# Kernel tuning notes

Hardware: AMD Instinct MI355X
Metric: run time of the kernel (lower is better)

Reference implementation:

```python
import jax, jax.numpy as jnp
import numpy as np

N0, N1 = 20000, 20000     # users, items
F0 = 512                  # raw feature dim per type
HID = 64                  # hidden_dim == H * D
H, D = 8, 8               # num_heads, out_dim
P = 2                     # metapaths per side
E = 200000                # metapath instances per metapath
L = 3                     # metapath length (nodes)
B = 8192                  # link-prediction target batch
AV = 128                  # attn_vec_dim
CH = 128                  # ProductMLP hidden = max(128, HID//2)
ETYPES_USER = [[0, 1], [0, 1]]
ETYPES_ITEM = [[1, 0], [1, 0]]


def setup_inputs() -> dict:
    key = jax.random.key(0)
    ks = jax.random.split(key, 32)
    def nrm(k, shape, fan_in):
        return (jax.random.normal(k, shape, dtype=jnp.float32) * (1.414 / np.sqrt(fan_in))).astype(jnp.float32)
    inp = {}
    inp['feats0'] = jax.random.normal(ks[0], (N0, F0), dtype=jnp.float32)
    inp['feats1'] = jax.random.normal(ks[1], (N1, F0), dtype=jnp.float32)
    for t, off in ((0, 2), (1, 6)):
        inp[f'tower{t}_pw'] = nrm(ks[off], (F0, HID), F0)
        inp[f'tower{t}_pb'] = jnp.zeros((HID,), jnp.float32)
        inp[f'tower{t}_w2'] = nrm(ks[off + 1], (HID, HID), HID)
        inp[f'tower{t}_b2'] = jnp.zeros((HID,), jnp.float32)
        inp[f'tower{t}_g'] = jnp.ones((HID,), jnp.float32)
        inp[f'tower{t}_be'] = jnp.zeros((HID,), jnp.float32)
    inp['r_vec'] = jax.random.normal(ks[10], (2, HID // 2, 2), dtype=jnp.float32)
    inp['attn_user'] = nrm(ks[11], (P, H, D), D)
    inp['attn_item'] = nrm(ks[12], (P, H, D), D)
    inp['su_w1'] = nrm(ks[13], (HID, AV), HID)
    inp['su_b1'] = jnp.zeros((AV,), jnp.float32)
    inp['su_w2'] = nrm(ks[14], (AV,), AV)
    inp['si_w1'] = nrm(ks[15], (HID, AV), HID)
    inp['si_b1'] = jnp.zeros((AV,), jnp.float32)
    inp['si_w2'] = nrm(ks[16], (AV,), AV)
    inp['cw1'] = nrm(ks[17], (HID, CH), HID)
    inp['cb1'] = jnp.zeros((CH,), jnp.float32)
    inp['cw2'] = nrm(ks[18], (CH, 2), CH)
    inp['idx0'] = jnp.arange(N0, dtype=jnp.int32)
    inp['idx1'] = jnp.arange(N1, dtype=jnp.int32) + N0
    inp['emi_user'] = jax.random.randint(ks[20], (P, E, L), 0, N0 + N1, dtype=jnp.int32)
    inp['tgt_user'] = jax.random.randint(ks[21], (P, E), 0, B, dtype=jnp.int32)
    inp['emi_item'] = jax.random.randint(ks[22], (P, E, L), 0, N0 + N1, dtype=jnp.int32)
    inp['tgt_item'] = jax.random.randint(ks[23], (P, E), 0, B, dtype=jnp.int32)
    return inp


def _tower(x, pw, pb, w2, b2, g, be):
    # Linear -> GELU -> Linear -> residual -> LayerNorm (dropout off in eval)
    z = x @ pw + pb
    h = jax.nn.gelu(z, approximate=False)
    h = h @ w2 + b2
    y = h + z
    mu = y.mean(-1, keepdims=True)
    var = ((y - mu) ** 2).mean(-1, keepdims=True)
    return (y - mu) / jnp.sqrt(var + 1e-5) * g + be


def _rot_full(r_vec):
    # normalize to unit complex, then even etypes = r, odd etypes = conj(r)
    r = r_vec / jnp.linalg.norm(r_vec, axis=-1, keepdims=True)
    conj = r * jnp.array([1.0, -1.0], dtype=r.dtype)
    return jnp.stack([r, conj], axis=1).reshape(-1, r.shape[1], 2)  # [num_edge_type, HID//2, 2]


def _final_r(rfull, etypes):
    # cumulative complex rotation applied to each position along the metapath
    fr = [None] * L
    fr[L - 1] = jnp.stack([jnp.ones(HID // 2), jnp.zeros(HID // 2)], axis=1).astype(rfull.dtype)
    for i in range(L - 2, -1, -1):
        rv = rfull[etypes[i]]
        re = fr[i + 1][:, 0] * rv[:, 0] - fr[i + 1][:, 1] * rv[:, 1]
        im = fr[i + 1][:, 0] * rv[:, 1] + fr[i + 1][:, 1] * rv[:, 0]
        fr[i] = jnp.stack([re, im], axis=1)
    return jnp.stack(fr)  # [L, HID//2, 2]


def _metapath(feat, emi, tgt, attn, etypes, rfull):
    # gather node features along each metapath instance: [E, L, HID//2, 2]
    ed = feat[emi].reshape(emi.shape[0], L, HID // 2, 2)
    fr = _final_r(rfull, etypes)  # last position is identity rotation
    re = ed[..., 0] * fr[:, :, 0] - ed[..., 1] * fr[:, :, 1]
    im = ed[..., 0] * fr[:, :, 1] + ed[..., 1] * fr[:, :, 0]
    hidden = jnp.stack([re, im], -1).mean(axis=1).reshape(-1, HID)  # mean over metapath positions
    eft = hidden.reshape(-1, H, D)
    e = jax.nn.leaky_relu((eft * attn).sum(-1), 0.01)  # [E, H]
    # edge softmax over instances sharing a target node
    m = jax.ops.segment_max(e, tgt, num_segments=B)
    m = jnp.where(jnp.isfinite(m), m, 0.0)
    a = jnp.exp(e - m[tgt])
    s = jax.ops.segment_sum(a, tgt, num_segments=B)
    w = a / (s[tgt] + 1e-9)
    ret = jax.ops.segment_sum(w[..., None] * eft, tgt, num_segments=B)  # [B, H, D]
    return jax.nn.elu(ret.reshape(B, HID))


def _semantic(outs, w1, b1, w2):
    hs = jnp.stack(outs)  # [P, B, HID]
    s = (jnp.tanh(hs @ w1 + b1) @ w2).mean(axis=1)  # [P]
    beta = jax.nn.softmax(s)
    return (beta[:, None, None] * hs).sum(0)  # [B, HID]


def reference(feats0, feats1, tower0_pw, tower0_pb, tower0_w2, tower0_b2, tower0_g, tower0_be,
              tower1_pw, tower1_pb, tower1_w2, tower1_b2, tower1_g, tower1_be,
              r_vec, attn_user, attn_item, su_w1, su_b1, su_w2, si_w1, si_b1, si_w2,
              cw1, cb1, cw2, idx0, idx1, emi_user, tgt_user, emi_item, tgt_item):
    t0 = _tower(feats0, tower0_pw, tower0_pb, tower0_w2, tower0_b2, tower0_g, tower0_be)
    t1 = _tower(feats1, tower1_pw, tower1_pb, tower1_w2, tower1_b2, tower1_g, tower1_be)
    feat = jnp.zeros((N0 + N1, HID), jnp.float32).at[idx0].set(t0).at[idx1].set(t1)
    rfull = _rot_full(r_vec)
    user_outs = [_metapath(feat, emi_user[p], tgt_user[p], attn_user[p], ETYPES_USER[p], rfull) for p in range(P)]
    item_outs = [_metapath(feat, emi_item[p], tgt_item[p], attn_item[p], ETYPES_ITEM[p], rfull) for p in range(P)]
    h_user = _semantic(user_outs, su_w1, su_b1, su_w2)
    h_item = _semantic(item_outs, si_w1, si_b1, si_w2)
    x = h_user * h_item
    h = jax.nn.relu(x @ cw1 + cb1)
    logits = h @ cw2
    return jax.nn.softmax(logits, axis=-1)
```

## Files before the change

kernel.cpp:

```cpp
#include <hip/hip_runtime.h>
#include <hip/hip_bf16.h>
#include <math.h>

#define NN0 20000
#define NN1 20000
#define NTOT 40000
#define FF0 512
#define HIDD 64
#define EEE 200000
#define BBB 8192
#define AVV 128
#define CHH 128

typedef __bf16 bf16x8 __attribute__((ext_vector_type(8)));
typedef __bf16 bf16x4 __attribute__((ext_vector_type(4)));
typedef float f32x4 __attribute__((ext_vector_type(4)));
typedef float f32x2 __attribute__((ext_vector_type(2)));

__device__ __forceinline__ float fast_tanh(float x) {
    float e2 = __expf(2.f * x);
    return 1.f - 2.f / (e2 + 1.f);
}

__device__ __forceinline__ f32x2 bf2_to_f32x2(unsigned int c) {
    f32x2 r;
    r.x = __uint_as_float(c << 16);
    r.y = __uint_as_float(c & 0xffff0000u);
    return r;
}

__global__ __launch_bounds__(256) void prep_hist(
    const float* __restrict__ pw0, const float* __restrict__ pw1,
    const float* __restrict__ w20, const float* __restrict__ w21,
    __bf16* __restrict__ wprep, __bf16* __restrict__ w2prep,
    const int* __restrict__ tgt_user, const int* __restrict__ tgt_item,
    int* __restrict__ cnt)
{
    int bx = blockIdx.x;
    if (bx < 16) {
        int tw = bx & 1, seg = bx >> 1;
        const float* w = tw ? pw1 : pw0;
        __bf16* base = wprep + tw * 65536;
        for (int idx = seg * 4096 + threadIdx.x; idx < (seg + 1) * 4096; idx += 256) {
            int k = idx >> 6, n = idx & 63;
            float v = w[idx];
            __bf16 hi = (__bf16)v;
            __bf16 lo = (__bf16)(v - (float)hi);
            int ks = k >> 5, kb = (k >> 3) & 3, j = k & 7;
            int nt = n >> 4, fr = n & 15;
            int lane = kb * 16 + fr;
            int off = ((ks * 4 + nt) * 64 + lane) * 8 + j;
            base[off] = hi;
            base[32768 + off] = lo;
        }
        const float* w2 = tw ? w21 : w20;
        __bf16* base2 = w2prep + tw * 8192;
        for (int idx = seg * 512 + threadIdx.x; idx < (seg + 1) * 512; idx += 256) {
            int k = idx >> 6, n = idx & 63;
            float v = w2[idx];
            __bf16 hi = (__bf16)v;
            __bf16 lo = (__bf16)(v - (float)hi);
            int ks = k >> 5, kb = (k >> 3) & 3, j = k & 7;
            int nt = n >> 4, fr = n & 15;
            int lane = kb * 16 + fr;
            int off = ((ks * 4 + nt) * 64 + lane) * 8 + j;
            base2[off] = hi;
            base2[4096 + off] = lo;
        }
    } else {
        int flat = bx - 16;
        int combo = flat & 3, blk = flat >> 2;
        const int* tgt = (combo < 2 ? tgt_user : tgt_item) + (long)(combo & 1) * EEE;
        int i = blk * 256 + threadIdx.x;
        if (i < EEE) atomicAdd(&cnt[combo * BBB + tgt[i]], 1);
    }
}

__global__ __launch_bounds__(256) void scan_kernel(const int* __restrict__ cnt, int* __restrict__ offs,
                                                   int* __restrict__ cur32, float* __restrict__ s_acc)
{
    int pth = blockIdx.x;
    if (pth == 0 && threadIdx.x < 4) s_acc[threadIdx.x] = 0.f;
    const int* c = cnt + pth * BBB;
    int* o = offs + pth * (BBB + 1);
    __shared__ int part[256];
    int tid = threadIdx.x;
    int base = tid * 32;
    int local[32];
    int sum = 0;
    for (int j = 0; j < 32; j++) { local[j] = sum; sum += c[base + j]; }
    part[tid] = sum;
    __syncthreads();
    for (int d = 1; d < 256; d <<= 1) {
        int v = (tid >= d) ? part[tid - d] : 0;
        __syncthreads();
        part[tid] += v;
        __syncthreads();
    }
    int pre = (tid == 0) ? 0 : part[tid - 1];
    for (int j = 0; j < 32; j++) {
        int val = pre + local[j];
        o[base + j] = val;
        if (((base + j) & 255) == 0) cur32[pth * 32 + ((base + j) >> 8)] = val;
    }
    if (tid == 255) o[BBB] = pre + sum;
}

#define CHUNKF 1024
__global__ __launch_bounds__(128) void tower_binA(
    const float* __restrict__ x0, const float* __restrict__ x1,
    const __bf16* __restrict__ wprep, const __bf16* __restrict__ w2prep,
    const float* __restrict__ pb0, const float* __restrict__ pb1,
    const float* __restrict__ b20, const float* __restrict__ b21,
    const float* __restrict__ g0, const float* __restrict__ g1,
    const float* __restrict__ be0, const float* __restrict__ be1,
    const int* __restrict__ idxa, const int* __restrict__ idxb,
    __hip_bfloat16* __restrict__ feat,
    const int* __restrict__ tgt_user, const int* __restrict__ tgt_item,
    const int* __restrict__ emi_user, const int* __restrict__ emi_item,
    int* __restrict__ cur32, ushort4* __restrict__ binbuf)
{
    __shared__ __align__(16) char pool[8960];
    int bx = blockIdx.x;
    if (bx < 2500) {
        int tile = bx >> 1, tw = bx & 1;
        const float* x  = tw ? x1 : x0;
        const float* pb = tw ? pb1 : pb0;
        const float* b2 = tw ? b21 : b20;
        const float* g  = tw ? g1 : g0;
        const float* be = tw ? be1 : be0;
        const int* idx  = tw ? idxb : idxa;
        float (*hs)[68] = (float(*)[68])pool;
        float* pq  = (float*)(pool + 4352);
        float* pq2 = (float*)(pool + 4480);

        int wv = threadIdx.x >> 6;
        int l = threadIdx.x & 63;
        int fr = l & 15, kb = l >> 4;
        int nt0 = 2 * wv;
        int row0 = tile * 16;
        const float* xp = x + (long)(row0 + fr) * FF0 + kb * 8;
        const __bf16* bp = wprep + tw * 65536;

        f32x4 acc[2];
#pragma unroll
        for (int n2 = 0; n2 < 2; n2++) acc[n2] = (f32x4){0.f, 0.f, 0.f, 0.f};

        float4 a0c, a1c, a0n, a1n;
        bf16x8 bhc[2], blc[2], bhn[2], bln[2];

        a0c = *(const float4*)xp;
        a1c = *(const float4*)(xp + 4);
#pragma unroll
        for (int n2 = 0; n2 < 2; n2++) {
            bhc[n2] = *(const bf16x8*)(bp + ((nt0 + n2) * 64 + l) * 8);
            blc[n2] = *(const bf16x8*)(bp + 32768 + ((nt0 + n2) * 64 + l) * 8);
        }

#pragma unroll 2
        for (int ks = 0; ks < 16; ks++) {
            if (ks + 1 < 16) {
                a0n = *(const float4*)(xp + (ks + 1) * 32);
                a1n = *(const float4*)(xp + (ks + 1) * 32 + 4);
#pragma unroll
                for (int n2 = 0; n2 < 2; n2++) {
                    bhn[n2] = *(const bf16x8*)(bp + (((ks + 1) * 4 + nt0 + n2) * 64 + l) * 8);
                    bln[n2] = *(const bf16x8*)(bp + 32768 + (((ks + 1) * 4 + nt0 + n2) * 64 + l) * 8);
                }
            }
            float av[8] = {a0c.x, a0c.y, a0c.z, a0c.w, a1c.x, a1c.y, a1c.z, a1c.w};
            bf16x8 ah, al;
#pragma unroll
            for (int j = 0; j < 8; j++) {
                __bf16 h = (__bf16)av[j];
                ah[j] = h;
                al[j] = (__bf16)(av[j] - (float)h);
            }
#pragma unroll
            for (int n2 = 0; n2 < 2; n2++) {
                acc[n2] = __builtin_amdgcn_mfma_f32_16x16x32_bf16(ah, bhc[n2], acc[n2], 0, 0, 0);
                acc[n2] = __builtin_amdgcn_mfma_f32_16x16x32_bf16(al, bhc[n2], acc[n2], 0, 0, 0);
                acc[n2] = __builtin_amdgcn_mfma_f32_16x16x32_bf16(ah, blc[n2], acc[n2], 0, 0, 0);
            }
            a0c = a0n; a1c = a1n;
#pragma unroll
            for (int n2 = 0; n2 < 2; n2++) { bhc[n2] = bhn[n2]; blc[n2] = bln[n2]; }
        }

        float pbv[2], b2v[2];
#pragma unroll
        for (int n2 = 0; n2 < 2; n2++) {
            pbv[n2] = pb[(nt0 + n2) * 16 + fr];
            b2v[n2] = b2[(nt0 + n2) * 16 + fr];
        }
        f32x4 acc2[2];
#pragma unroll
        for (int n2 = 0; n2 < 2; n2++) {
#pragma unroll
            for (int j = 0; j < 4; j++) {
                float z = acc[n2][j] + pbv[n2];
                float h = 0.5f * z * (1.f + erff(z * 0.70710678118654752f));
                hs[kb * 4 + j][(nt0 + n2) * 16 + fr] = h;
                acc2[n2][j] = z + b2v[n2];
            }
        }
        __syncthreads();

        const __bf16* w2p = w2prep + tw * 8192;
#pragma unroll
        for (int ks = 0; ks < 2; ks++) {
            float4 h0 = *(const float4*)&hs[fr][ks * 32 + kb * 8];
            float4 h1 = *(const float4*)&hs[fr][ks * 32 + kb * 8 + 4];
            float hv[8] = {h0.x, h0.y, h0.z, h0.w, h1.x, h1.y, h1.z, h1.w};
            bf16x8 ah, al;
#pragma unroll
            for (int j = 0; j < 8; j++) {
                __bf16 h = (__bf16)hv[j];
                ah[j] = h;
                al[j] = (__bf16)(hv[j] - (float)h);
            }
#pragma unroll
            for (int n2 = 0; n2 < 2; n2++) {
                bf16x8 bh2 = *(const bf16x8*)(w2p + ((ks * 4 + nt0 + n2) * 64 + l) * 8);
                bf16x8 bl2 = *(const bf16x8*)(w2p + 4096 + ((ks * 4 + nt0 + n2) * 64 + l) * 8);
                acc2[n2] = __builtin_amdgcn_mfma_f32_16x16x32_bf16(ah, bh2, acc2[n2], 0, 0, 0);
                acc2[n2] = __builtin_amdgcn_mfma_f32_16x16x32_bf16(al, bh2, acc2[n2], 0, 0, 0);
                acc2[n2] = __builtin_amdgcn_mfma_f32_16x16x32_bf16(ah, bl2, acc2[n2], 0, 0, 0);
            }
        }

        float pj[4];
#pragma unroll
        for (int j = 0; j < 4; j++) {
            float p = acc2[0][j] + acc2[1][j];
            p += __shfl_xor(p, 1); p += __shfl_xor(p, 2);
            p += __shfl_xor(p, 4); p += __shfl_xor(p, 8);
            pj[j] = p;
        }
        if (fr == 0) {
#pragma unroll
            for (int j = 0; j < 4; j++) pq[wv * 16 + kb * 4 + j] = pj[j];
        }
        __syncthreads();
        float mu[4];
#pragma unroll
        for (int j = 0; j < 4; j++)
            mu[j] = (pj[j] + pq[(wv ^ 1) * 16 + kb * 4 + j]) * (1.f / 64.f);
        float d[2][4], vj[4];
#pragma unroll
        for (int j = 0; j < 4; j++) {
            d[0][j] = acc2[0][j] - mu[j];
            d[1][j] = acc2[1][j] - mu[j];
            float v = d[0][j] * d[0][j] + d[1][j] * d[1][j];
            v += __shfl_xor(v, 1); v += __shfl_xor(v, 2);
            v += __shfl_xor(v, 4); v += __shfl_xor(v, 8);
            vj[j] = v;
        }
        if (fr == 0) {
#pragma unroll
            for (int j = 0; j < 4; j++) pq2[wv * 16 + kb * 4 + j] = vj[j];
        }
        __syncthreads();
        float gv[2], bev[2];
#pragma unroll
        for (int n2 = 0; n2 < 2; n2++) {
            gv[n2] = g[(nt0 + n2) * 16 + fr];
            bev[n2] = be[(nt0 + n2) * 16 + fr];
        }
#pragma unroll
        for (int j = 0; j < 4; j++) {
            float var = (vj[j] + pq2[(wv ^ 1) * 16 + kb * 4 + j]) * (1.f / 64.f);
            float is = 1.f / sqrtf(var + 1e-5f);
#pragma unroll
            for (int n2 = 0; n2 < 2; n2++)
                hs[kb * 4 + j][(nt0 + n2) * 16 + fr] = d[n2][j] * is * gv[n2] + bev[n2];
        }
        __syncthreads();
#pragma unroll
        for (int r = 0; r < 8; r++) {
            int rr = wv * 8 + r;
            feat[(long)idx[row0 + rr] * HIDD + l] = __float2bfloat16(hs[rr][l]);
        }
    } else {
        int flat = bx - 2500;
        int combo = flat & 3;
        int base = (flat >> 2) * CHUNKF;
        const int* tgt = (combo < 2 ? tgt_user : tgt_item) + (long)(combo & 1) * EEE;
        const int* emi = (combo < 2 ? emi_user : emi_item) + (long)(combo & 1) * EEE * 3;
        ushort4* sbuf = (ushort4*)pool;
        int* lcnt  = (int*)(pool + 8192);
        int* lofs  = lcnt + 32;
        int* gbase = lofs + 33;
        int* lcur  = gbase + 32;
        int tid = threadIdx.x;
        if (tid < 32) { lcnt[tid] = 0; lcur[tid] = 0; }
        __syncthreads();
        ushort4 ent[8]; int bk[8];
#pragma unroll
        for (int ps = 0; ps < 8; ps++) {
            int i = base + ps * 128 + tid;
            if (i < EEE) {
                int t = tgt[i];
                ent[ps] = make_ushort4((unsigned short)emi[3 * i], (unsigned short)emi[3 * i + 1],
                                       (unsigned short)emi[3 * i + 2], (unsigned short)t);
                bk[ps] = t >> 8;
                atomicAdd(&lcnt[bk[ps]], 1);
            } else bk[ps] = -1;
        }
        __syncthreads();
        if (tid == 0) {
            int run = 0;
            for (int k = 0; k < 32; k++) { lofs[k] = run; run += lcnt[k]; }
            lofs[32] = run;
        }
        __syncthreads();
        if (tid < 32) gbase[tid] = atomicAdd(&cur32[combo * 32 + tid], lcnt[tid]);
        __syncthreads();
#pragma unroll
        for (int ps = 0; ps < 8; ps++) {
            if (bk[ps] >= 0) {
                int pos = lofs[bk[ps]] + atomicAdd(&lcur[bk[ps]], 1);
                sbuf[pos] = ent[ps];
            }
        }
        __syncthreads();
        int total = lofs[32];
        ushort4* dst = binbuf + (long)combo * EEE;
        for (int j = tid; j < total; j += 128) {
            ushort4 e = sbuf[j];
            int k = e.w >> 8;
            dst[gbase[k] + (j - lofs[k])] = e;
        }
    }
}

#define BKCAP 7680
__global__ __launch_bounds__(256) void binB_kernel(
    const int* __restrict__ offs,
    const ushort4* __restrict__ binbuf, ushort4* __restrict__ nodes)
{
    int combo = blockIdx.y;
    int k = blockIdx.x;
    const int* of = offs + combo * (BBB + 1);
    int rbeg = of[k << 8], rend = of[(k + 1) << 8];
    int cnt = rend - rbeg;
    if (cnt > BKCAP) cnt = BKCAP;
    __shared__ ushort4 sbuf[BKCAP];
    __shared__ int lh[256];
    __shared__ int part[256];
    int tid = threadIdx.x;
    lh[tid] = 0;
    __syncthreads();
    const ushort4* src = binbuf + (long)combo * EEE + rbeg;
    for (int j = tid; j < cnt; j += 256)
        atomicAdd(&lh[src[j].w & 255], 1);
    __syncthreads();
    int myc = lh[tid];
    part[tid] = myc;
    __syncthreads();
    for (int d = 1; d < 256; d <<= 1) {
        int u = (tid >= d) ? part[tid - d] : 0;
        __syncthreads();
        part[tid] += u;
        __syncthreads();
    }
    int myofs = part[tid] - myc;
    __syncthreads();
    lh[tid] = myofs;
    part[tid] = 0;
    __syncthreads();
    for (int j = tid; j < cnt; j += 256) {
        ushort4 e = src[j];
        int b = e.w & 255;
        int pos = lh[b] + atomicAdd(&part[b], 1);
        if (pos < BKCAP) sbuf[pos] = e;
    }
    __syncthreads();
    ushort4* dst = nodes + (long)combo * EEE + rbeg;
    for (int j = tid; j < cnt; j += 256) dst[j] = sbuf[j];
}

__global__ __launch_bounds__(256) void flash_mp(
    const __hip_bfloat16* __restrict__ feat, const ushort4* __restrict__ nodes,
    const int* __restrict__ offs, const float* __restrict__ r_vec,
    const float* __restrict__ attn_user, const float* __restrict__ attn_item,
    float* __restrict__ ret)
{
    int combo = blockIdx.y;
    int wid = threadIdx.x >> 6, lane = threadIdx.x & 63;
    int half = lane >> 5, p = lane & 31;
    int side = combo >> 1;
    const float* attn = (side == 0 ? attn_user : attn_item) + (combo & 1) * 64;
    const unsigned int* f2 = (const unsigned int*)feat;
    float2 rb = ((const float2*)r_vec)[p];
    float invn = 1.f / sqrtf(rb.x * rb.x + rb.y * rb.y);
    float rvx = rb.x * invn, rvy = rb.y * invn;
    if (side == 0) rvy = -rvy;
    float aRe = attn[2 * p], aIm = attn[2 * p + 1];
    f32x2 av  = { aRe * (1.f / 3.f), aIm * (1.f / 3.f) };
    f32x2 apv = { (rvx * aRe + rvy * aIm) * (1.f / 3.f),
                  (rvx * aIm - rvy * aRe) * (1.f / 3.f) };
    int t = blockIdx.x * 4 + wid;
    const int* of = offs + combo * (BBB + 1);
    int beg = of[t], end = of[t + 1];
    int n = end - beg;
    const ushort4* nd = nodes + (long)combo * EEE;

    float m = -3.4e38f, s = 0.f;
    f32x2 A02 = {0.f, 0.f}, A1 = {0.f, 0.f};

    unsigned int c0[4], c1[4], c2[4];
    ushort4 nq[4];
    if (n > 0) {
#pragma unroll
        for (int q = 0; q < 4; q++) {
            ushort4 a = nd[min(beg + 2 * q + half, EEE - 1)];
            c0[q] = f2[(int)a.x * 32 + p];
            c1[q] = f2[(int)a.y * 32 + p];
            c2[q] = f2[(int)a.z * 32 + p];
        }
#pragma unroll
        for (int q = 0; q < 4; q++)
            nq[q] = nd[min(beg + 8 + 2 * q + half, EEE - 1)];
    }
    for (int it = 0; it < n; it += 8) {
        f32x2 u1[4], v02[4];
        float e[4];
#pragma unroll
        for (int q = 0; q < 4; q++) {
            f32x2 u0 = bf2_to_f32x2(c0[q]);
            u1[q]    = bf2_to_f32x2(c1[q]);
            f32x2 u2 = bf2_to_f32x2(c2[q]);
            v02[q] = u0 + u2;
        }
        if (it + 8 < n) {
#pragma unroll
            for (int q = 0; q < 4; q++) {
                c0[q] = f2[(int)nq[q].x * 32 + p];
                c1[q] = f2[(int)nq[q].y * 32 + p];
                c2[q] = f2[(int)nq[q].z * 32 + p];
            }
#pragma unroll
            for (int q = 0; q < 4; q++)
                nq[q] = nd[min(beg + it + 16 + 2 * q + half, EEE - 1)];
        }
#pragma unroll
        for (int q = 0; q < 4; q++) {
            f32x2 tt = v02[q] * av + u1[q] * apv;
            float pa = tt.x + tt.y;
            pa += __shfl_xor(pa, 1);
            pa += __shfl_xor(pa, 2);
            e[q] = fmaxf(pa, 0.01f * pa);
        }
        if (it + 8 > n) {
#pragma unroll
            for (int q = 0; q < 4; q++)
                if (it + 2 * q + half >= n) e[q] = -3.4e38f;
        }
        float mx = fmaxf(fmaxf(e[0], e[1]), fmaxf(e[2], e[3]));
        float mn = fmaxf(m, fmaxf(mx, __shfl_xor(mx, 32)));
        float alpha = __expf(m - mn);
        s *= alpha; A02 *= alpha; A1 *= alpha;
        float wl = 0.f;
#pragma unroll
        for (int q = 0; q < 4; q++) {
            float w = __expf(e[q] - mn);
            wl += w;
            A02 += v02[q] * w;
            A1  += u1[q] * w;
        }
        s += wl + __shfl_xor(wl, 32);
        m = mn;
    }
    float Sx = A02.x + __shfl_xor(A02.x, 32);
    float Sy = A02.y + __shfl_xor(A02.y, 32);
    float Tx = A1.x + __shfl_xor(A1.x, 32);
    float Ty = A1.y + __shfl_xor(A1.y, 32);
    float inv = (1.f / 3.f) / (s + 1e-9f);
    float vx = (Sx + rvx * Tx - rvy * Ty) * inv;
    float vy = (Sy + rvx * Ty + rvy * Tx) * inv;
    vx = vx > 0.f ? vx : __expf(vx) - 1.f;
    vy = vy > 0.f ? vy : __expf(vy) - 1.f;
    if (half == 0)
        ((float2*)ret)[((long)combo * BBB + t) * 32 + p] = make_float2(vx, vy);
}

__global__ __launch_bounds__(256) void sem_kernel(
    const float* __restrict__ ret,
    const float* __restrict__ su_w1, const float* __restrict__ su_b1, const float* __restrict__ su_w2,
    const float* __restrict__ si_w1, const float* __restrict__ si_b1, const float* __restrict__ si_w2,
    float* __restrict__ s_acc)
{
    int combo = blockIdx.y;
    int side = combo >> 1;
    const float* w1 = side ? si_w1 : su_w1;
    const float* b1 = side ? si_b1 : su_b1;
    const float* w2 = side ? si_w2 : su_w2;
    __shared__ float vs[64][68];
    __shared__ float w1s[64][128];
    int tid = threadIdx.x;
    int rowbase = blockIdx.x * 64;
    const float4* r4 = (const float4*)ret;
    for (int li = tid; li < 1024; li += 256) {
        int r = li >> 4, c4 = li & 15;
        float4 v = r4[((long)combo * BBB + rowbase + r) * 16 + c4];
        *(float4*)&vs[r][c4 * 4] = v;
    }
    const float4* w14 = (const float4*)w1;
    for (int li = tid; li < 2048; li += 256) {
        float4 v = w14[li];
        *(float4*)&w1s[li >> 5][(li & 31) * 4] = v;
    }
    __syncthreads();
    int ct = tid & 15, rt = tid >> 4;
    float acc[4][8];
#pragma unroll
    for (int cc = 0; cc < 8; cc++) {
        float b = b1[8 * ct + cc];
#pragma unroll
        for (int j = 0; j < 4; j++) acc[j][cc] = b;
    }
    for (int k = 0; k < 64; k += 4) {
        float4 xv[4];
#pragma unroll
        for (int j = 0; j < 4; j++) xv[j] = *(const float4*)&vs[4 * rt + j][k];
#pragma unroll
        for (int kk = 0; kk < 4; kk++) {
            float4 wv0 = *(const float4*)&w1s[k + kk][8 * ct];
            float4 wv1 = *(const float4*)&w1s[k + kk][8 * ct + 4];
#pragma unroll
            for (int j = 0; j < 4; j++) {
                float xx = kk == 0 ? xv[j].x : kk == 1 ? xv[j].y : kk == 2 ? xv[j].z : xv[j].w;
                acc[j][0] = fmaf(xx, wv0.x, acc[j][0]);
                acc[j][1] = fmaf(xx, wv0.y, acc[j][1]);
                acc[j][2] = fmaf(xx, wv0.z, acc[j][2]);
                acc[j][3] = fmaf(xx, wv0.w, acc[j][3]);
                acc[j][4] = fmaf(xx, wv1.x, acc[j][4]);
                acc[j][5] = fmaf(xx, wv1.y, acc[j][5]);
                acc[j][6] = fmaf(xx, wv1.z, acc[j][6]);
                acc[j][7] = fmaf(xx, wv1.w, acc[j][7]);
            }
        }
    }
    float tot = 0.f;
#pragma unroll
    for (int cc = 0; cc < 8; cc++) {
        float w2v = w2[8 * ct + cc];
#pragma unroll
        for (int j = 0; j < 4; j++) tot += fast_tanh(acc[j][cc]) * w2v;
    }
    for (int off = 32; off; off >>= 1) tot += __shfl_xor(tot, off);
    __shared__ float red[4];
    int lane = tid & 63, wid = tid >> 6;
    if (lane == 0) red[wid] = tot;
    __syncthreads();
    if (tid == 0) atomicAdd(&s_acc[combo], red[0] + red[1] + red[2] + red[3]);
}

__global__ __launch_bounds__(256) void final_kernel(
    const float* __restrict__ ret, const float* __restrict__ s_acc,
    const float* __restrict__ cw1, const float* __restrict__ cb1, const float* __restrict__ cw2,
    float* __restrict__ outp)
{
    float s0 = s_acc[0] * (1.f / BBB), s1 = s_acc[1] * (1.f / BBB);
    float s2 = s_acc[2] * (1.f / BBB), s3 = s_acc[3] * (1.f / BBB);
    float mu = fmaxf(s0, s1);
    float e0 = __expf(s0 - mu), e1 = __expf(s1 - mu);
    float bu0 = e0 / (e0 + e1), bu1 = e1 / (e0 + e1);
    float mi = fmaxf(s2, s3);
    float f0 = __expf(s2 - mi), f1 = __expf(s3 - mi);
    float bi0 = f0 / (f0 + f1), bi1 = f1 / (f0 + f1);

    __shared__ float xsld[64][68];
    __shared__ float w1s[64][128];
    int tid = threadIdx.x;
    int rowbase = blockIdx.x * 64;
    const float4* r4 = (const float4*)ret;
    for (int li = tid; li < 1024; li += 256) {
        int r = li >> 4, c4 = li & 15;
        float4 a = r4[((long)0 * BBB + rowbase + r) * 16 + c4];
        float4 b = r4[((long)1 * BBB + rowbase + r) * 16 + c4];
        float4 cc = r4[((long)2 * BBB + rowbase + r) * 16 + c4];
        float4 d = r4[((long)3 * BBB + rowbase + r) * 16 + c4];
        float4 xv;
        xv.x = (bu0 * a.x + bu1 * b.x) * (bi0 * cc.x + bi1 * d.x);
        xv.y = (bu0 * a.y + bu1 * b.y) * (bi0 * cc.y + bi1 * d.y);
        xv.z = (bu0 * a.z + bu1 * b.z) * (bi0 * cc.z + bi1 * d.z);
        xv.w = (bu0 * a.w + bu1 * b.w) * (bi0 * cc.w + bi1 * d.w);
        *(float4*)&xsld[r][c4 * 4] = xv;
    }
    const float4* w14 = (const float4*)cw1;
    for (int li = tid; li < 2048; li += 256) {
        float4 v = w14[li];
        *(float4*)&w1s[li >> 5][(li & 31) * 4] = v;
    }
    __syncthreads();
    int ct = tid & 15, rt = tid >> 4;
    float acc[4][8];
#pragma unroll
    for (int cc = 0; cc < 8; cc++) {
        float b = cb1[8 * ct + cc];
#pragma unroll
        for (int j = 0; j < 4; j++) acc[j][cc] = b;
    }
    for (int k = 0; k < 64; k += 4) {
        float4 xv[4];
#pragma unroll
        for (int j = 0; j < 4; j++) xv[j] = *(const float4*)&xsld[4 * rt + j][k];
#pragma unroll
        for (int kk = 0; kk < 4; kk++) {
            float4 wv0 = *(const float4*)&w1s[k + kk][8 * ct];
            float4 wv1 = *(const float4*)&w1s[k + kk][8 * ct + 4];
#pragma unroll
            for (int j = 0; j < 4; j++) {
                float xx = kk == 0 ? xv[j].x : kk == 1 ? xv[j].y : kk == 2 ? xv[j].z : xv[j].w;
                acc[j][0] = fmaf(xx, wv0.x, acc[j][0]);
                acc[j][1] = fmaf(xx, wv0.y, acc[j][1]);
                acc[j][2] = fmaf(xx, wv0.z, acc[j][2]);
                acc[j][3] = fmaf(xx, wv0.w, acc[j][3]);
                acc[j][4] = fmaf(xx, wv1.x, acc[j][4]);
                acc[j][5] = fmaf(xx, wv1.y, acc[j][5]);
                acc[j][6] = fmaf(xx, wv1.z, acc[j][6]);
                acc[j][7] = fmaf(xx, wv1.w, acc[j][7]);
            }
        }
    }
    float pp0[4], pp1[4];
#pragma unroll
    for (int j = 0; j < 4; j++) { pp0[j] = 0.f; pp1[j] = 0.f; }
#pragma unroll
    for (int cc = 0; cc < 8; cc++) {
        int col = 8 * ct + cc;
        float c0 = cw2[col * 2], c1 = cw2[col * 2 + 1];
#pragma unroll
        for (int j = 0; j < 4; j++) {
            float h = fmaxf(acc[j][cc], 0.f);
            pp0[j] = fmaf(h, c0, pp0[j]);
            pp1[j] = fmaf(h, c1, pp1[j]);
        }
    }
    __syncthreads();
    float2* red = (float2*)xsld;
#pragma unroll
    for (int j = 0; j < 4; j++)
        red[(4 * rt + j) * 16 + ct] = make_float2(pp0[j], pp1[j]);
    __syncthreads();
    if (tid < 64) {
        float q0 = 0.f, q1 = 0.f;
        for (int i = 0; i < 16; i++) {
            float2 e = red[tid * 16 + i];
            q0 += e.x; q1 += e.y;
        }
        float mx = fmaxf(q0, q1);
        float a0 = __expf(q0 - mx), a1 = __expf(q1 - mx);
        float dn = a0 + a1;
        outp[(rowbase + tid) * 2] = a0 / dn;
        outp[(rowbase + tid) * 2 + 1] = a1 / dn;
    }
}

extern "C" void kernel_launch(void* const* d_in, const int* in_sizes, int n_in,
                              void* d_out, int out_size, void* d_ws, size_t ws_size,
                              hipStream_t stream)
{
    const float* feats0 = (const float*)d_in[0];
    const float* feats1 = (const float*)d_in[1];
    const float* t0_pw = (const float*)d_in[2];
    const float* t0_pb = (const float*)d_in[3];
    const float* t0_w2 = (const float*)d_in[4];
    const float* t0_b2 = (const float*)d_in[5];
    const float* t0_g  = (const float*)d_in[6];
    const float* t0_be = (const float*)d_in[7];
    const float* t1_pw = (const float*)d_in[8];
    const float* t1_pb = (const float*)d_in[9];
    const float* t1_w2 = (const float*)d_in[10];
    const float* t1_b2 = (const float*)d_in[11];
    const float* t1_g  = (const float*)d_in[12];
    const float* t1_be = (const float*)d_in[13];
    const float* r_vec = (const float*)d_in[14];
    const float* attn_user = (const float*)d_in[15];
    const float* attn_item = (const float*)d_in[16];
    const float* su_w1 = (const float*)d_in[17];
    const float* su_b1 = (const float*)d_in[18];
    const float* su_w2 = (const float*)d_in[19];
    const float* si_w1 = (const float*)d_in[20];
    const float* si_b1 = (const float*)d_in[21];
    const float* si_w2 = (const float*)d_in[22];
    const float* cw1 = (const float*)d_in[23];
    const float* cb1 = (const float*)d_in[24];
    const float* cw2 = (const float*)d_in[25];
    const int* idx0 = (const int*)d_in[26];
    const int* idx1 = (const int*)d_in[27];
    const int* emi_user = (const int*)d_in[28];
    const int* tgt_user = (const int*)d_in[29];
    const int* emi_item = (const int*)d_in[30];
    const int* tgt_item = (const int*)d_in[31];
    float* outp = (float*)d_out;

    char* ws = (char*)d_ws;
    __hip_bfloat16* feat = (__hip_bfloat16*)(ws + 0);
    int*     cnt    = (int*)(ws + 5120000);
    int*     cur32  = (int*)(ws + 5382144);
    int*     offs   = (int*)(ws + 5382656);
    float*   s_acc  = (float*)(ws + 5513984);
    ushort4* binbuf = (ushort4*)(ws + 5514240);
    ushort4* nodes  = (ushort4*)(ws + 11914240);
    float*   ret_buf= (float*)(ws + 18314240);
    __bf16*  wprep  = (__bf16*)(ws + 26702848);
    __bf16*  w2prep = (__bf16*)(ws + 11914240);

    hipMemsetAsync(cnt, 0, 4 * BBB * sizeof(int), stream);

    prep_hist<<<16 + 4 * ((EEE + 255) / 256), 256, 0, stream>>>(
        t0_pw, t1_pw, t0_w2, t1_w2, wprep, w2prep, tgt_user, tgt_item, cnt);

    scan_kernel<<<4, 256, 0, stream>>>(cnt, offs, cur32, s_acc);

    tower_binA<<<2500 + 4 * ((EEE + CHUNKF - 1) / CHUNKF), 128, 0, stream>>>(
        feats0, feats1, wprep, w2prep, t0_pb, t1_pb,
        t0_b2, t1_b2, t0_g, t1_g, t0_be, t1_be, idx0, idx1, feat,
        tgt_user, tgt_item, emi_user, emi_item, cur32, binbuf);

    binB_kernel<<<dim3(32, 4), 256, 0, stream>>>(offs, binbuf, nodes);

    flash_mp<<<dim3(BBB / 4, 4), 256, 0, stream>>>(feat, nodes, offs, r_vec,
                                                   attn_user, attn_item, ret_buf);

    sem_kernel<<<dim3(BBB / 64, 4), 256, 0, stream>>>(ret_buf, su_w1, su_b1, su_w2,
                                                      si_w1, si_b1, si_w2, s_acc);
    final_kernel<<<BBB / 64, 256, 0, stream>>>(ret_buf, s_acc, cw1, cb1, cw2, outp);
}
```

Before: 327.8 us.

## Replace fine histogram and scan kernel with coarse bucket counts and in-kernel prefixes

New measurement: 292.5 us. 1.12x faster.

```diff
diff --git a/kernel.cpp b/kernel.cpp
--- a/kernel.cpp
+++ b/kernel.cpp
@@ -29,13 +29,27 @@
     return r;
 }
 
+__device__ __forceinline__ void coarse_prefix(const int* __restrict__ cnt32p, int combo, int tid,
+                                              int& cv, int& excl) {
+    cv = cnt32p[(combo * 32 + tid) * 32];
+    int pre = cv;
+#pragma unroll
+    for (int d = 1; d < 32; d <<= 1) {
+        int o = __shfl_up(pre, d);
+        if (tid >= d) pre += o;
+    }
+    excl = pre - cv;
+}
+
+#define HCHUNK 1024
 __global__ __launch_bounds__(256) void prep_hist(
     const float* __restrict__ pw0, const float* __restrict__ pw1,
     const float* __restrict__ w20, const float* __restrict__ w21,
     __bf16* __restrict__ wprep, __bf16* __restrict__ w2prep,
     const int* __restrict__ tgt_user, const int* __restrict__ tgt_item,
-    int* __restrict__ cnt)
+    int* __restrict__ cnt32p)
 {
+    __shared__ int ch[32];
     int bx = blockIdx.x;
     if (bx < 16) {
         int tw = bx & 1, seg = bx >> 1;
@@ -71,39 +85,18 @@
         int flat = bx - 16;
         int combo = flat & 3, blk = flat >> 2;
         const int* tgt = (combo < 2 ? tgt_user : tgt_item) + (long)(combo & 1) * EEE;
-        int i = blk * 256 + threadIdx.x;
-        if (i < EEE) atomicAdd(&cnt[combo * BBB + tgt[i]], 1);
-    }
-}
-
-__global__ __launch_bounds__(256) void scan_kernel(const int* __restrict__ cnt, int* __restrict__ offs,
-                                                   int* __restrict__ cur32, float* __restrict__ s_acc)
-{
-    int pth = blockIdx.x;
-    if (pth == 0 && threadIdx.x < 4) s_acc[threadIdx.x] = 0.f;
-    const int* c = cnt + pth * BBB;
-    int* o = offs + pth * (BBB + 1);
-    __shared__ int part[256];
-    int tid = threadIdx.x;
-    int base = tid * 32;
-    int local[32];
-    int sum = 0;
-    for (int j = 0; j < 32; j++) { local[j] = sum; sum += c[base + j]; }
-    part[tid] = sum;
-    __syncthreads();
-    for (int d = 1; d < 256; d <<= 1) {
-        int v = (tid >= d) ? part[tid - d] : 0;
-        __syncthreads();
-        part[tid] += v;
-        __syncthreads();
-    }
-    int pre = (tid == 0) ? 0 : part[tid - 1];
-    for (int j = 0; j < 32; j++) {
-        int val = pre + local[j];
-        o[base + j] = val;
-        if (((base + j) & 255) == 0) cur32[pth * 32 + ((base + j) >> 8)] = val;
-    }
-    if (tid == 255) o[BBB] = pre + sum;
+        int tid = threadIdx.x;
+        if (tid < 32) ch[tid] = 0;
+        __syncthreads();
+        int base = blk * HCHUNK;
+#pragma unroll
+        for (int q = 0; q < 4; q++) {
+            int i = base + q * 256 + tid;
+            if (i < EEE) atomicAdd(&ch[tgt[i] >> 8], 1);
+        }
+        __syncthreads();
+        if (tid < 32 && ch[tid]) atomicAdd(&cnt32p[(combo * 32 + tid) * 32], ch[tid]);
+    }
 }
 
 #define CHUNKF 1024
@@ -118,7 +111,8 @@
     __hip_bfloat16* __restrict__ feat,
     const int* __restrict__ tgt_user, const int* __restrict__ tgt_item,
     const int* __restrict__ emi_user, const int* __restrict__ emi_item,
-    int* __restrict__ cur32, ushort4* __restrict__ binbuf)
+    const int* __restrict__ cnt32p, int* __restrict__ cur32cnt,
+    ushort4* __restrict__ binbuf)
 {
     __shared__ __align__(16) char pool[8960];
     int bx = blockIdx.x;
@@ -168,6 +162,7 @@
                     bln[n2] = *(const bf16x8*)(bp + 32768 + (((ks + 1) * 4 + nt0 + n2) * 64 + l) * 8);
                 }
             }
+            __builtin_amdgcn_sched_barrier(0);
             float av[8] = {a0c.x, a0c.y, a0c.z, a0c.w, a1c.x, a1c.y, a1c.z, a1c.w};
             bf16x8 ah, al;
 #pragma unroll
@@ -314,7 +309,11 @@
             lofs[32] = run;
         }
         __syncthreads();
-        if (tid < 32) gbase[tid] = atomicAdd(&cur32[combo * 32 + tid], lcnt[tid]);
+        if (tid < 32) {
+            int cv, excl;
+            coarse_prefix(cnt32p, combo, tid, cv, excl);
+            gbase[tid] = excl + atomicAdd(&cur32cnt[combo * 32 + tid], lcnt[tid]);
+        }
         __syncthreads();
 #pragma unroll
         for (int ps = 0; ps < 8; ps++) {
@@ -336,21 +335,27 @@
 
 #define BKCAP 7680
 __global__ __launch_bounds__(256) void binB_kernel(
-    const int* __restrict__ offs,
+    const int* __restrict__ cnt32p, int* __restrict__ offs,
     const ushort4* __restrict__ binbuf, ushort4* __restrict__ nodes)
 {
     int combo = blockIdx.y;
     int k = blockIdx.x;
-    const int* of = offs + combo * (BBB + 1);
-    int rbeg = of[k << 8], rend = of[(k + 1) << 8];
-    int cnt = rend - rbeg;
-    if (cnt > BKCAP) cnt = BKCAP;
     __shared__ ushort4 sbuf[BKCAP];
     __shared__ int lh[256];
     __shared__ int part[256];
+    __shared__ int cex[32], ccn[32];
     int tid = threadIdx.x;
+    if (tid < 32) {
+        int cv, excl;
+        coarse_prefix(cnt32p, combo, tid, cv, excl);
+        cex[tid] = excl;
+        ccn[tid] = cv;
+    }
     lh[tid] = 0;
     __syncthreads();
+    int rbeg = cex[k];
+    int cnt = ccn[k];
+    if (cnt > BKCAP) cnt = BKCAP;
     const ushort4* src = binbuf + (long)combo * EEE + rbeg;
     for (int j = tid; j < cnt; j += 256)
         atomicAdd(&lh[src[j].w & 255], 1);
@@ -365,6 +370,8 @@
         __syncthreads();
     }
     int myofs = part[tid] - myc;
+    offs[combo * (BBB + 1) + (k << 8) + tid] = rbeg + myofs;
+    if (k == 31 && tid == 0) offs[combo * (BBB + 1) + BBB] = EEE;
     __syncthreads();
     lh[tid] = myofs;
     part[tid] = 0;
@@ -699,29 +706,27 @@
 
     char* ws = (char*)d_ws;
     __hip_bfloat16* feat = (__hip_bfloat16*)(ws + 0);
-    int*     cnt    = (int*)(ws + 5120000);
-    int*     cur32  = (int*)(ws + 5382144);
-    int*     offs   = (int*)(ws + 5382656);
-    float*   s_acc  = (float*)(ws + 5513984);
-    ushort4* binbuf = (ushort4*)(ws + 5514240);
-    ushort4* nodes  = (ushort4*)(ws + 11914240);
-    float*   ret_buf= (float*)(ws + 18314240);
-    __bf16*  wprep  = (__bf16*)(ws + 26702848);
-    __bf16*  w2prep = (__bf16*)(ws + 11914240);
-
-    hipMemsetAsync(cnt, 0, 4 * BBB * sizeof(int), stream);
-
-    prep_hist<<<16 + 4 * ((EEE + 255) / 256), 256, 0, stream>>>(
-        t0_pw, t1_pw, t0_w2, t1_w2, wprep, w2prep, tgt_user, tgt_item, cnt);
-
-    scan_kernel<<<4, 256, 0, stream>>>(cnt, offs, cur32, s_acc);
+    int*     cnt32p  = (int*)(ws + 5120000);
+    int*     cur32cnt= (int*)(ws + 5136384);
+    float*   s_acc   = (float*)(ws + 5136896);
+    int*     offs    = (int*)(ws + 5137408);
+    ushort4* binbuf  = (ushort4*)(ws + 5268736);
+    ushort4* nodes   = (ushort4*)(ws + 11668736);
+    float*   ret_buf = (float*)(ws + 18068736);
+    __bf16*  wprep   = (__bf16*)(ws + 26457344);
+    __bf16*  w2prep  = (__bf16*)(ws + 11668736);
+
+    hipMemsetAsync(cnt32p, 0, 16384 + 512 + 256, stream);
+
+    prep_hist<<<16 + 4 * ((EEE + HCHUNK - 1) / HCHUNK), 256, 0, stream>>>(
+        t0_pw, t1_pw, t0_w2, t1_w2, wprep, w2prep, tgt_user, tgt_item, cnt32p);
 
     tower_binA<<<2500 + 4 * ((EEE + CHUNKF - 1) / CHUNKF), 128, 0, stream>>>(
         feats0, feats1, wprep, w2prep, t0_pb, t1_pb,
         t0_b2, t1_b2, t0_g, t1_g, t0_be, t1_be, idx0, idx1, feat,
-        tgt_user, tgt_item, emi_user, emi_item, cur32, binbuf);
-
-    binB_kernel<<<dim3(32, 4), 256, 0, stream>>>(offs, binbuf, nodes);
+        tgt_user, tgt_item, emi_user, emi_item, cnt32p, cur32cnt, binbuf);
+
+    binB_kernel<<<dim3(32, 4), 256, 0, stream>>>(cnt32p, offs, binbuf, nodes);
 
     flash_mp<<<dim3(BBB / 4, 4), 256, 0, stream>>>(feat, nodes, offs, r_vec,
                                                    attn_user, attn_item, ret_buf);
```
